# Optimization experiments

Hardware: AMD Instinct MI355X
Metric: run time of the kernel (lower is better)

The kernel has to match this reference:

```python
import jax, jax.numpy as jnp
import numpy as np

NEG_SLOPE = 0.2
BN_EPS = 1e-5


def gat_conv(x, W_src, W_dst, att_src, att_dst, bias, src, dst, num_nodes):
    # PyG GATConv, heads=1, concat=True, self-loops already included in (src,dst)
    h_src = x @ W_src                      # [N, H]
    h_dst = x @ W_dst                      # [N, H]
    a_src = h_src @ att_src                # [N]
    a_dst = h_dst @ att_dst                # [N]
    e = jax.nn.leaky_relu(a_src[src] + a_dst[dst], NEG_SLOPE)   # [E]
    # segment softmax over incoming edges of each dst node
    m = jax.ops.segment_max(e, dst, num_segments=num_nodes)     # [N]
    p = jnp.exp(e - m[dst])
    denom = jax.ops.segment_sum(p, dst, num_segments=num_nodes) # [N]
    alpha = p / denom[dst]                                      # [E]
    msgs = alpha[:, None] * h_src[src]                           # [E, H]
    out = jax.ops.segment_sum(msgs, dst, num_segments=num_nodes)
    return out + bias


def setup_inputs() -> dict:
    key = jax.random.key(0)
    ks = jax.random.split(key, 20)
    N, D_IN, H1, H2, FC, C = 100000, 256, 128, 128, 64, 40
    E = 1600000
    inp = {}
    inp['x'] = jax.random.normal(ks[0], (N, D_IN), dtype=jnp.float32)
    inp['edge_index'] = jax.random.randint(ks[1], (2, E), 0, N, dtype=jnp.int64)
    s = 1.0 / np.sqrt(D_IN)
    inp['W1_src'] = jax.random.uniform(ks[2], (D_IN, H1), jnp.float32, -s, s)
    inp['W1_dst'] = jax.random.uniform(ks[3], (D_IN, H1), jnp.float32, -s, s)
    inp['att1_src'] = jax.random.normal(ks[4], (H1,), jnp.float32) * 0.1
    inp['att1_dst'] = jax.random.normal(ks[5], (H1,), jnp.float32) * 0.1
    inp['b1'] = jnp.zeros((H1,), jnp.float32)
    s = 1.0 / np.sqrt(H1)
    inp['W2_src'] = jax.random.uniform(ks[6], (H1, H2), jnp.float32, -s, s)
    inp['W2_dst'] = jax.random.uniform(ks[7], (H1, H2), jnp.float32, -s, s)
    inp['att2_src'] = jax.random.normal(ks[8], (H2,), jnp.float32) * 0.1
    inp['att2_dst'] = jax.random.normal(ks[9], (H2,), jnp.float32) * 0.1
    inp['b2'] = jnp.zeros((H2,), jnp.float32)
    s = 1.0 / np.sqrt(H2)
    inp['fc1_w'] = jax.random.uniform(ks[10], (H2, FC), jnp.float32, -s, s)
    inp['fc1_b'] = jax.random.uniform(ks[11], (FC,), jnp.float32, -s, s)
    inp['gamma'] = jnp.ones((FC,), jnp.float32)
    inp['beta'] = jnp.zeros((FC,), jnp.float32)
    s = 1.0 / np.sqrt(FC)
    inp['fc2_w'] = jax.random.uniform(ks[12], (FC, C), jnp.float32, -s, s)
    inp['fc2_b'] = jax.random.uniform(ks[13], (C,), jnp.float32, -s, s)
    return inp


def reference(x, edge_index, W1_src, W1_dst, att1_src, att1_dst, b1,
              W2_src, W2_dst, att2_src, att2_dst, b2,
              fc1_w, fc1_b, gamma, beta, fc2_w, fc2_b):
    N = x.shape[0]
    loops = jnp.arange(N, dtype=edge_index.dtype)
    src = jnp.concatenate([edge_index[0], loops])
    dst = jnp.concatenate([edge_index[1], loops])
    h = jax.nn.relu(gat_conv(x, W1_src, W1_dst, att1_src, att1_dst, b1, src, dst, N))
    h = jax.nn.relu(gat_conv(h, W2_src, W2_dst, att2_src, att2_dst, b2, src, dst, N))
    h = h @ fc1_w + fc1_b                   # [N, 64]
    mu = jnp.mean(h, axis=0)
    var = jnp.var(h, axis=0)
    h = (h - mu) * jax.lax.rsqrt(var + BN_EPS) * gamma + beta
    h = jax.nn.relu(h)
    h = h @ fc2_w + fc2_b                   # [N, C]
    return jax.nn.log_softmax(h, axis=-1)
```

## Files before the change

### kernel.cpp

```cpp
#include <hip/hip_runtime.h>
#include <cstddef>

#define LSLOPE 0.2f
#define BN_EPS 1e-5f

__device__ __forceinline__ float lrelu(float x) { return x > 0.f ? x : LSLOPE * x; }

using half4 = __attribute__((ext_vector_type(4))) _Float16;
using half8 = __attribute__((ext_vector_type(8))) _Float16;
using f32x4 = __attribute__((ext_vector_type(4))) float;

struct h2 { _Float16 h, l; };
__device__ __forceinline__ h2 split2h(float x) {
  h2 r;
  r.h = (_Float16)x;
  r.l = (_Float16)(x - (float)r.h);
  return r;
}

__device__ __forceinline__ unsigned short f2bf(float x) {
  unsigned u = __float_as_uint(x);
  unsigned r = (u + 0x7fffu + ((u >> 16) & 1u)) >> 16;
  return (unsigned short)r;
}
__device__ __forceinline__ float bflo(unsigned int u) { return __uint_as_float(u << 16); }
__device__ __forceinline__ float bfhi(unsigned int u) { return __uint_as_float(u & 0xffff0000u); }

__device__ __forceinline__ void bfrag_body(const float* __restrict__ B, _Float16* __restrict__ bh,
                                           _Float16* __restrict__ bl, int K, int M, int t) {
  int KB = K >> 5;
  int lane = t & 63;
  int ckb  = t >> 6;
  int c  = ckb / KB, kb = ckb % KB;
  int mr = lane & 15, quad = lane >> 4;
  int col = c * 16 + mr;
  size_t obase = (size_t)t * 8;
#pragma unroll
  for (int j = 0; j < 8; ++j) {
    int k = kb * 32 + quad * 8 + j;
    h2 s = split2h(B[(size_t)k * M + col]);
    bh[obase + j] = s.h;
    bl[obase + j] = s.l;
  }
}

__device__ __forceinline__ void matvec_body(const float* __restrict__ A, const float* __restrict__ v,
                                            float* __restrict__ out, int R, int K, int t) {
  int w = t >> 6;
  int lane = t & 63;
  if (w >= R) return;
  const float* row = A + (size_t)w * K;
  float s = 0.f;
  for (int k = lane; k < K; k += 64) s = fmaf(row[k], v[k], s);
#pragma unroll
  for (int off = 32; off; off >>= 1) s += __shfl_xor(s, off, 64);
  if (lane == 0) out[w] = s;
}

__global__ __launch_bounds__(256) void prep_k(const float* __restrict__ W1s, const float* __restrict__ W2s,
                                              const float* __restrict__ fc1w,
                                              const float* __restrict__ W1d, const float* __restrict__ att1d,
                                              const float* __restrict__ W2d, const float* __restrict__ att2d,
                                              const float* __restrict__ att1s, const float* __restrict__ att2s,
                                              _Float16* B1h, _Float16* B1l, _Float16* B2h, _Float16* B2l,
                                              _Float16* Bfh, _Float16* Bfl,
                                              float* wvd1, float* wvd2, float* wvs1, float* wvs2) {
  int b = blockIdx.x;
  int tid = threadIdx.x;
  if (b < 16)       bfrag_body(W1s, B1h, B1l, 256, 128, b * 256 + tid);
  else if (b < 24)  bfrag_body(W2s, B2h, B2l, 128, 128, (b - 16) * 256 + tid);
  else if (b < 28)  bfrag_body(fc1w, Bfh, Bfl, 128, 64, (b - 24) * 256 + tid);
  else if (b < 92)  matvec_body(W1d, att1d, wvd1, 256, 128, (b - 28) * 256 + tid);
  else if (b < 124) matvec_body(W2d, att2d, wvd2, 128, 128, (b - 92) * 256 + tid);
  else if (b < 188) matvec_body(W1s, att1s, wvs1, 256, 128, (b - 124) * 256 + tid);
  else              matvec_body(W2s, att2s, wvs2, 128, 128, (b - 188) * 256 + tid);
}

template<int K, int MCOLS, bool PS>
__global__ __launch_bounds__(256) void gemm_dk(const float* __restrict__ Af,
                                               const _Float16* __restrict__ Ah,
                                               const _Float16* __restrict__ Al,
                                               const _Float16* __restrict__ Bh,
                                               const _Float16* __restrict__ Bl,
                                               float* __restrict__ Cf,
                                               unsigned short* __restrict__ Cbf,
                                               const float* __restrict__ wvs,
                                               float* __restrict__ asrc,
                                               const float* __restrict__ wvd,
                                               float* __restrict__ adout,
                                               int N,
                                               const float* __restrict__ bias) {
  constexpr int KB   = K / 32;
  constexpr int HALF = MCOLS / 2;
  constexpr int CT   = HALF / 16;
  const int tid  = threadIdx.x;
  const int wv   = tid >> 6;
  const int wm   = wv >> 1;
  const int wn   = wv & 1;
  const int lane = tid & 63;
  const int quad = lane >> 4;
  const int mr   = lane & 15;
  const int row0 = blockIdx.x * 64;

  int rowr[2];
  bool rok[2];
#pragma unroll
  for (int r = 0; r < 2; ++r) {
    rowr[r] = row0 + wm * 32 + r * 16 + mr;
    rok[r]  = rowr[r] < N;
  }

  f32x4 acc[2][CT];
#pragma unroll
  for (int r = 0; r < 2; ++r)
#pragma unroll
    for (int c = 0; c < CT; ++c) acc[r][c] = (f32x4){0.f, 0.f, 0.f, 0.f};
  float pas[2] = {0.f, 0.f}, pad[2] = {0.f, 0.f};

  const size_t cstride = (size_t)KB * 512;
  const _Float16* bbh = Bh + (size_t)(wn * CT) * cstride + (size_t)lane * 8;
  const _Float16* bbl = Bl + (size_t)(wn * CT) * cstride + (size_t)lane * 8;
  const float4 zf4 = make_float4(0.f, 0.f, 0.f, 0.f);
  const half8 hz = {(_Float16)0, (_Float16)0, (_Float16)0, (_Float16)0,
                    (_Float16)0, (_Float16)0, (_Float16)0, (_Float16)0};

#pragma unroll
  for (int kb = 0; kb < KB; ++kb) {
    const int kk = kb * 32;
    half8 ah[2], al[2];
#pragma unroll
    for (int r = 0; r < 2; ++r) {
      if (PS) {
        const size_t go = (size_t)rowr[r] * K + kk + quad * 8;
        ah[r] = rok[r] ? *(const half8*)&Ah[go] : hz;
        al[r] = rok[r] ? *(const half8*)&Al[go] : hz;
      } else {
        const float* ap = Af + (size_t)rowr[r] * K + kk + quad * 8;
        float4 f0 = rok[r] ? *(const float4*)ap : zf4;
        float4 f1 = rok[r] ? *(const float4*)(ap + 4) : zf4;
        h2 s0 = split2h(f0.x), s1 = split2h(f0.y), s2 = split2h(f0.z), s3 = split2h(f0.w);
        h2 s4 = split2h(f1.x), s5 = split2h(f1.y), s6 = split2h(f1.z), s7 = split2h(f1.w);
        half8 h, l;
        h[0] = s0.h; h[1] = s1.h; h[2] = s2.h; h[3] = s3.h;
        h[4] = s4.h; h[5] = s5.h; h[6] = s6.h; h[7] = s7.h;
        l[0] = s0.l; l[1] = s1.l; l[2] = s2.l; l[3] = s3.l;
        l[4] = s4.l; l[5] = s5.l; l[6] = s6.l; l[7] = s7.l;
        ah[r] = h;
        al[r] = l;
      }
    }
    if (wn == 0 && (wvs || wvd)) {
#pragma unroll
      for (int j = 0; j < 8; ++j) {
        const float vs = wvs ? wvs[kk + quad * 8 + j] : 0.f;
        const float vd = wvd ? wvd[kk + quad * 8 + j] : 0.f;
#pragma unroll
        for (int r = 0; r < 2; ++r) {
          const float av = (float)ah[r][j] + (float)al[r][j];
          if (wvs) pas[r] = fmaf(av, vs, pas[r]);
          if (wvd) pad[r] = fmaf(av, vd, pad[r]);
        }
      }
    }
#pragma unroll
    for (int c = 0; c < CT; ++c) {
      const half8 bh = *(const half8*)&bbh[(size_t)kb * 512 + (size_t)c * cstride];
      const half8 bl = *(const half8*)&bbl[(size_t)kb * 512 + (size_t)c * cstride];
#pragma unroll
      for (int r = 0; r < 2; ++r) {
        f32x4 a = acc[r][c];
        a = __builtin_amdgcn_mfma_f32_16x16x32_f16(al[r], bh, a, 0, 0, 0);
        a = __builtin_amdgcn_mfma_f32_16x16x32_f16(ah[r], bl, a, 0, 0, 0);
        a = __builtin_amdgcn_mfma_f32_16x16x32_f16(ah[r], bh, a, 0, 0, 0);
        acc[r][c] = a;
      }
    }
  }

#pragma unroll
  for (int r = 0; r < 2; ++r)
#pragma unroll
    for (int c = 0; c < CT; ++c) {
      const int gcol = wn * HALF + c * 16 + mr;
      const float bv = bias ? bias[gcol] : 0.f;
#pragma unroll
      for (int q = 0; q < 4; ++q) {
        const int grow = row0 + wm * 32 + r * 16 + quad * 4 + q;
        if (grow < N) {
          float val = acc[r][c][q] + bv;
          if (Cf)  Cf[(size_t)grow * MCOLS + gcol] = val;
          if (Cbf) Cbf[(size_t)grow * 128 + gcol] = f2bf(val);
        }
      }
    }
  if (wn == 0 && wvs) {
#pragma unroll
    for (int r = 0; r < 2; ++r) {
      float d = pas[r];
      d += __shfl_xor(d, 16, 64);
      d += __shfl_xor(d, 32, 64);
      const int grow = row0 + wm * 32 + r * 16 + mr;
      if (quad == 0 && grow < N) asrc[grow] = d;
    }
  }
  if (wn == 0 && wvd) {
#pragma unroll
    for (int r = 0; r < 2; ++r) {
      float d = pad[r];
      d += __shfl_xor(d, 16, 64);
      d += __shfl_xor(d, 32, 64);
      const int grow = row0 + wm * 32 + r * 16 + mr;
      if (quad == 0 && grow < N) adout[grow] = d;
    }
  }
}

__global__ void deg_count_k(const int* __restrict__ edst, int E, int N, int* __restrict__ deg) {
  int i = blockIdx.x * 256 + threadIdx.x;
  if (i >= E + N) return;
  int d = (i < E) ? edst[i] : (i - E);
  atomicAdd(&deg[d], 1);
}

__global__ __launch_bounds__(1024) void scan1_k(const int* __restrict__ deg, int n,
                                                int* __restrict__ ex, int* __restrict__ bsum) {
  __shared__ int sm[1024];
  int t = threadIdx.x;
  int idx = blockIdx.x * 1024 + t;
  int v = (idx < n) ? deg[idx] : 0;
  sm[t] = v;
  __syncthreads();
  for (int off = 1; off < 1024; off <<= 1) {
    int tv = (t >= off) ? sm[t - off] : 0;
    __syncthreads();
    sm[t] += tv;
    __syncthreads();
  }
  if (idx < n) ex[idx] = sm[t] - v;
  if (t == 1023) bsum[blockIdx.x] = sm[t];
}

__global__ void scan3_k(int* __restrict__ ex, const int* __restrict__ bsum, int n, int nb, int total,
                        int* __restrict__ cursor) {
  __shared__ int pbase[2];
  int idx = blockIdx.x * 256 + threadIdx.x;
  int bin0 = (blockIdx.x * 256) >> 10;
  if (threadIdx.x < 2) {
    int b = bin0 + threadIdx.x;
    int s = 0;
    for (int i = 0; i < b && i < nb; ++i) s += bsum[i];
    pbase[threadIdx.x] = s;
  }
  __syncthreads();
  if (idx < n) {
    int v = ex[idx] + pbase[(idx >> 10) - bin0];
    ex[idx] = v;
    cursor[idx] = v;
  }
  if (idx == 0) ex[n] = total;
}

__global__ void scatter_range_k(const int* __restrict__ esrc, const int* __restrict__ edst,
                                int E, int N, int d0, int d1,
                                int* __restrict__ cursor, int* __restrict__ csr_src) {
  int i = blockIdx.x * 256 + threadIdx.x;
  if (i >= E + N) return;
  int d = (i < E) ? edst[i] : (i - E);
  if (d < d0 || d >= d1) return;
  int s = (i < E) ? esrc[i] : d;
  int pos = atomicAdd(&cursor[d], 1);
  csr_src[pos] = s;
}

__global__ __launch_bounds__(256) void gat_agg_k(const unsigned short* __restrict__ hbf,
                                                 const float* __restrict__ a_src,
                                                 const float* __restrict__ a_dst, const int* __restrict__ rowstart,
                                                 const int* __restrict__ csr_src, const float* __restrict__ bias,
                                                 _Float16* __restrict__ oh, _Float16* __restrict__ ol,
                                                 const float* __restrict__ wvd, float* __restrict__ ad_out,
                                                 int N) {
  int w = (blockIdx.x * blockDim.x + threadIdx.x) >> 6;
  int lane = threadIdx.x & 63;
  if (w >= N) return;
  int s0 = rowstart[w];
  int s1 = rowstart[w + 1];
  int deg = s1 - s0;
  float ad = a_dst[w];

  int sA = 0;
  float eA = -3.0e38f;
  if (lane < deg) {
    sA = csr_src[s0 + lane];
    eA = lrelu(a_src[sA] + ad);
  }
  float m = eA;
  for (int j = s0 + 64 + lane; j < s1; j += 64) {
    int s = csr_src[j];
    m = fmaxf(m, lrelu(a_src[s] + ad));
  }
#pragma unroll
  for (int off = 32; off; off >>= 1) m = fmaxf(m, __shfl_xor(m, off, 64));

  float preg = (lane < deg) ? __expf(eA - m) : 0.f;
  float den = preg;
  for (int j = s0 + 64 + lane; j < s1; j += 64) {
    int s = csr_src[j];
    den += __expf(lrelu(a_src[s] + ad) - m);
  }
#pragma unroll
  for (int off = 32; off; off >>= 1) den += __shfl_xor(den, off, 64);
  float inv = 1.f / den;

  const int q  = lane >> 4;
  const int sl = lane & 15;
  const uint4* hrow4 = (const uint4*)hbf;
  float acc[8];
#pragma unroll
  for (int i = 0; i < 8; ++i) acc[i] = 0.f;

  int lim  = deg < 64 ? deg : 64;
  int lim4 = (lim + 3) & ~3;
  for (int jj = 0; jj < lim4; jj += 4) {
    int e = jj + q;
    int s = __shfl(sA, e, 64);
    float wgt = __shfl(preg, e, 64) * inv;
    uint4 u = hrow4[(size_t)s * 16 + sl];
    acc[0] = fmaf(wgt, bflo(u.x), acc[0]);
    acc[1] = fmaf(wgt, bfhi(u.x), acc[1]);
    acc[2] = fmaf(wgt, bflo(u.y), acc[2]);
    acc[3] = fmaf(wgt, bfhi(u.y), acc[3]);
    acc[4] = fmaf(wgt, bflo(u.z), acc[4]);
    acc[5] = fmaf(wgt, bfhi(u.z), acc[5]);
    acc[6] = fmaf(wgt, bflo(u.w), acc[6]);
    acc[7] = fmaf(wgt, bfhi(u.w), acc[7]);
  }
  for (int j = s0 + 64 + q; j < s1; j += 4) {
    int s = csr_src[j];
    float wgt = __expf(lrelu(a_src[s] + ad) - m) * inv;
    uint4 u = hrow4[(size_t)s * 16 + sl];
    acc[0] = fmaf(wgt, bflo(u.x), acc[0]);
    acc[1] = fmaf(wgt, bfhi(u.x), acc[1]);
    acc[2] = fmaf(wgt, bflo(u.y), acc[2]);
    acc[3] = fmaf(wgt, bfhi(u.y), acc[3]);
    acc[4] = fmaf(wgt, bflo(u.z), acc[4]);
    acc[5] = fmaf(wgt, bfhi(u.z), acc[5]);
    acc[6] = fmaf(wgt, bflo(u.w), acc[6]);
    acc[7] = fmaf(wgt, bfhi(u.w), acc[7]);
  }
#pragma unroll
  for (int i = 0; i < 8; ++i) {
    acc[i] += __shfl_xor(acc[i], 16, 64);
    acc[i] += __shfl_xor(acc[i], 32, 64);
  }
  if (q == 0) {
    float4 b0 = *(const float4*)&bias[8 * sl];
    float4 b1 = *(const float4*)&bias[8 * sl + 4];
    float v[8];
    v[0] = fmaxf(acc[0] + b0.x, 0.f);
    v[1] = fmaxf(acc[1] + b0.y, 0.f);
    v[2] = fmaxf(acc[2] + b0.z, 0.f);
    v[3] = fmaxf(acc[3] + b0.w, 0.f);
    v[4] = fmaxf(acc[4] + b1.x, 0.f);
    v[5] = fmaxf(acc[5] + b1.y, 0.f);
    v[6] = fmaxf(acc[6] + b1.z, 0.f);
    v[7] = fmaxf(acc[7] + b1.w, 0.f);
    half8 vh, vl;
#pragma unroll
    for (int i = 0; i < 8; ++i) {
      h2 s = split2h(v[i]);
      vh[i] = s.h;
      vl[i] = s.l;
    }
    size_t base = (size_t)w * 128 + 8 * sl;
    *(half8*)&oh[base] = vh;
    *(half8*)&ol[base] = vl;
    if (wvd) {
      float4 w0 = *(const float4*)&wvd[8 * sl];
      float4 w1 = *(const float4*)&wvd[8 * sl + 4];
      float dd = v[0] * w0.x + v[1] * w0.y + v[2] * w0.z + v[3] * w0.w
               + v[4] * w1.x + v[5] * w1.y + v[6] * w1.z + v[7] * w1.w;
      dd += __shfl_xor(dd, 1, 64);
      dd += __shfl_xor(dd, 2, 64);
      dd += __shfl_xor(dd, 4, 64);
      dd += __shfl_xor(dd, 8, 64);
      if (sl == 0) ad_out[w] = dd;
    }
  }
}

__global__ __launch_bounds__(256) void bn_stats_k(const float* __restrict__ z, int N,
                                                  float* __restrict__ sums, float* __restrict__ sumsq) {
  __shared__ float ls[256], lq[256];
  int col = threadIdx.x & 63;
  int rg = threadIdx.x >> 6;
  float s = 0.f, q = 0.f;
  for (int r = blockIdx.x * 4 + rg; r < N; r += gridDim.x * 4) {
    float v = z[(size_t)r * 64 + col];
    s += v;
    q = fmaf(v, v, q);
  }
  ls[threadIdx.x] = s;
  lq[threadIdx.x] = q;
  __syncthreads();
  if (threadIdx.x < 64) {
    s = ls[col] + ls[col + 64] + ls[col + 128] + ls[col + 192];
    q = lq[col] + lq[col + 64] + lq[col + 128] + lq[col + 192];
    atomicAdd(&sums[col], s);
    atomicAdd(&sumsq[col], q);
  }
}

__global__ __launch_bounds__(256) void fc2_lsm_k(const float* __restrict__ z,
                                                 const float* __restrict__ sums, const float* __restrict__ sumsq,
                                                 const float* __restrict__ gamma, const float* __restrict__ beta,
                                                 const float* __restrict__ w,
                                                 const float* __restrict__ b, float* __restrict__ out,
                                                 int N, float invN) {
  __shared__ float ssc[64], ssh[64];
  if (threadIdx.x < 64) {
    int c = threadIdx.x;
    float mean = sums[c] * invN;
    float var = sumsq[c] * invN - mean * mean;
    float rs = rsqrtf(var + BN_EPS);
    float sc = gamma[c] * rs;
    ssc[c] = sc;
    ssh[c] = beta[c] - mean * sc;
  }
  __syncthreads();
  int n = blockIdx.x * 256 + threadIdx.x;
  if (n >= N) return;
  float o[40];
#pragma unroll
  for (int c = 0; c < 40; ++c) o[c] = b[c];
  const float* zr = z + (size_t)n * 64;
  for (int k = 0; k < 64; ++k) {
    float v = fmaxf(fmaf(zr[k], ssc[k], ssh[k]), 0.f);
#pragma unroll
    for (int c = 0; c < 40; ++c) o[c] = fmaf(v, w[k * 40 + c], o[c]);
  }
  float mx = o[0];
#pragma unroll
  for (int c = 1; c < 40; ++c) mx = fmaxf(mx, o[c]);
  float s = 0.f;
#pragma unroll
  for (int c = 0; c < 40; ++c) s += __expf(o[c] - mx);
  float ls = __logf(s);
  float* orow = out + (size_t)n * 40;
#pragma unroll
  for (int c = 0; c < 40; ++c) orow[c] = o[c] - mx - ls;
}

static inline char* al16(char* p) { return (char*)(((size_t)p + 15) & ~(size_t)15); }

extern "C" void kernel_launch(void* const* d_in, const int* in_sizes, int n_in,
                              void* d_out, int out_size, void* d_ws, size_t ws_size,
                              hipStream_t stream) {
  const float* x     = (const float*)d_in[0];
  const int*   eidx  = (const int*)d_in[1];
  const float* W1s   = (const float*)d_in[2];
  const float* W1d   = (const float*)d_in[3];
  const float* att1s = (const float*)d_in[4];
  const float* att1d = (const float*)d_in[5];
  const float* b1    = (const float*)d_in[6];
  const float* W2s   = (const float*)d_in[7];
  const float* W2d   = (const float*)d_in[8];
  const float* att2s = (const float*)d_in[9];
  const float* att2d = (const float*)d_in[10];
  const float* b2    = (const float*)d_in[11];
  const float* fc1w  = (const float*)d_in[12];
  const float* fc1b  = (const float*)d_in[13];
  const float* gamma = (const float*)d_in[14];
  const float* beta  = (const float*)d_in[15];
  const float* fc2w  = (const float*)d_in[16];
  const float* fc2b  = (const float*)d_in[17];
  float* out = (float*)d_out;

  const int N  = in_sizes[0] / 256;
  const int E  = in_sizes[1] / 2;
  const int ET = E + N;

  char* p = (char*)d_ws;
  int* deg      = (int*)p;     p += (size_t)N * 4;
  float* sums   = (float*)p;   p += 64 * 4;
  float* sumsq  = (float*)p;   p += 64 * 4;
  unsigned short* bhA = (unsigned short*)p; p += (size_t)N * 128 * 2;
  _Float16* hAh = (_Float16*)p;  p += (size_t)N * 128 * 2;
  _Float16* hAl = (_Float16*)p;  p += (size_t)N * 128 * 2;
  float* hF = (float*)p;         p += (size_t)N * 64 * 4;
  int* rowstart = (int*)p;     p += (size_t)(N + 1) * 4;
  int* cursor   = (int*)p;     p += (size_t)N * 4;
  int* csr_src  = (int*)p;     p += (size_t)ET * 4;
  float* a_src  = (float*)p;   p += (size_t)N * 4;
  float* a_dst  = (float*)p;   p += (size_t)N * 4;
  float* a_dst2 = (float*)p;   p += (size_t)N * 4;
  float* wvd1   = (float*)p;   p += 256 * 4;
  float* wvd2   = (float*)p;   p += 128 * 4;
  float* wvs1   = (float*)p;   p += 256 * 4;
  float* wvs2   = (float*)p;   p += 128 * 4;
  int* bsum     = (int*)p;     p += 256 * 4;
  p = al16(p);
  _Float16* B1h = (_Float16*)p; p += (size_t)256 * 128 * 2;
  _Float16* B1l = (_Float16*)p; p += (size_t)256 * 128 * 2;
  _Float16* B2h = (_Float16*)p; p += (size_t)128 * 128 * 2;
  _Float16* B2l = (_Float16*)p; p += (size_t)128 * 128 * 2;
  _Float16* Bfh = (_Float16*)p; p += (size_t)128 * 64 * 2;
  _Float16* Bfl = (_Float16*)p; p += (size_t)128 * 64 * 2;

  const int* esrc = eidx;
  const int* edst = eidx + E;

  hipMemsetAsync(deg, 0, (size_t)N * 4 + 512, stream);

  deg_count_k<<<(ET + 255) / 256, 256, 0, stream>>>(edst, E, N, deg);
  int nb = (N + 1023) / 1024;
  scan1_k<<<nb, 1024, 0, stream>>>(deg, N, rowstart, bsum);
  scan3_k<<<(N + 255) / 256, 256, 0, stream>>>(rowstart, bsum, N, nb, ET, cursor);
  {
    const int NR = 8;
    int step = (N + NR - 1) / NR;
    for (int r = 0; r < NR; ++r) {
      int d0 = r * step;
      int d1 = d0 + step < N ? d0 + step : N;
      scatter_range_k<<<(ET + 255) / 256, 256, 0, stream>>>(esrc, edst, E, N, d0, d1, cursor, csr_src);
    }
  }

  prep_k<<<220, 256, 0, stream>>>(W1s, W2s, fc1w, W1d, att1d, W2d, att2d, att1s, att2s,
                                  B1h, B1l, B2h, B2l, Bfh, Bfl, wvd1, wvd2, wvs1, wvs2);

  const int gdk = (N + 63) / 64;

  gemm_dk<256, 128, false><<<gdk, 256, 0, stream>>>(x, nullptr, nullptr, B1h, B1l,
                                                    nullptr, bhA, wvs1, a_src, wvd1, a_dst, N, nullptr);
  gat_agg_k<<<(N + 3) / 4, 256, 0, stream>>>(bhA, a_src, a_dst, rowstart, csr_src, b1,
                                             hAh, hAl, wvd2, a_dst2, N);

  gemm_dk<128, 128, true><<<gdk, 256, 0, stream>>>(nullptr, hAh, hAl, B2h, B2l,
                                                   nullptr, bhA, wvs2, a_src, nullptr, nullptr, N, nullptr);
  gat_agg_k<<<(N + 3) / 4, 256, 0, stream>>>(bhA, a_src, a_dst2, rowstart, csr_src, b2,
                                             hAh, hAl, nullptr, nullptr, N);

  gemm_dk<128, 64, true><<<gdk, 256, 0, stream>>>(nullptr, hAh, hAl, Bfh, Bfl,
                                                  hF, nullptr, nullptr, nullptr, nullptr, nullptr, N, fc1b);
  bn_stats_k<<<512, 256, 0, stream>>>(hF, N, sums, sumsq);
  fc2_lsm_k<<<(N + 255) / 256, 256, 0, stream>>>(hF, sums, sumsq, gamma, beta, fc2w, fc2b, out,
                                                 N, 1.0f / (float)N);
}
```

Baseline: 761.5 us.

## Stage A tiles through double-buffered LDS in dense GEMM kernels

The GEMM kernel now loads each 64x32 A tile cooperatively into shared memory, swizzled to avoid bank conflicts, instead of each wave reading its rows directly from global memory. Loads for the next k-block are issued into registers and written to a second LDS buffer while MFMAs run on the current one. For the fp32 first layer, the hi/lo fp16 split is also done once per element instead of by both column-half waves. This adds LDS traffic and a barrier per k-step, and the loop is no longer explicitly unrolled.

```diff
diff --git a/kernel.cpp b/kernel.cpp
--- a/kernel.cpp
+++ b/kernel.cpp
@@ -77,7 +77,7 @@
 }
 
 template<int K, int MCOLS, bool PS>
-__global__ __launch_bounds__(256) void gemm_dk(const float* __restrict__ Af,
+__global__ __launch_bounds__(256) void gemm_sk(const float* __restrict__ Af,
                                                const _Float16* __restrict__ Ah,
                                                const _Float16* __restrict__ Al,
                                                const _Float16* __restrict__ Bh,
@@ -93,22 +93,16 @@
   constexpr int KB   = K / 32;
   constexpr int HALF = MCOLS / 2;
   constexpr int CT   = HALF / 16;
+  __shared__ __align__(16) _Float16 sAh[2][64 * 32];
+  __shared__ __align__(16) _Float16 sAl[2][64 * 32];
   const int tid  = threadIdx.x;
+  const int row0 = blockIdx.x * 64;
   const int wv   = tid >> 6;
   const int wm   = wv >> 1;
   const int wn   = wv & 1;
   const int lane = tid & 63;
   const int quad = lane >> 4;
   const int mr   = lane & 15;
-  const int row0 = blockIdx.x * 64;
-
-  int rowr[2];
-  bool rok[2];
-#pragma unroll
-  for (int r = 0; r < 2; ++r) {
-    rowr[r] = row0 + wm * 32 + r * 16 + mr;
-    rok[r]  = rowr[r] < N;
-  }
 
   f32x4 acc[2][CT];
 #pragma unroll
@@ -116,38 +110,85 @@
 #pragma unroll
     for (int c = 0; c < CT; ++c) acc[r][c] = (f32x4){0.f, 0.f, 0.f, 0.f};
   float pas[2] = {0.f, 0.f}, pad[2] = {0.f, 0.f};
+
+  int srow, skc, soff;
+  bool sok;
+  if (PS) {
+    srow = tid >> 2;
+    skc  = (tid & 3) << 3;
+  } else {
+    srow = tid >> 3;
+    skc  = (tid & 7) << 2;
+  }
+  soff = srow * 32 + ((skc + srow * 8) & 31);
+  sok  = (row0 + srow) < N;
+  int srow2 = 0, skc2 = 0, soff2 = 0;
+  bool sok2 = false;
+  if (!PS) {
+    int s = tid + 256;
+    srow2 = s >> 3;
+    skc2  = (s & 7) << 2;
+    soff2 = srow2 * 32 + ((skc2 + srow2 * 8) & 31);
+    sok2  = (row0 + srow2) < N;
+  }
+
+  const float4 zf4 = make_float4(0.f, 0.f, 0.f, 0.f);
+  const uint4  zu4 = make_uint4(0u, 0u, 0u, 0u);
+
+  float4 pf0, pf1;
+  uint4 puh, pul;
+  if (PS) {
+    size_t go = (size_t)(row0 + srow) * K + skc;
+    puh = sok ? *(const uint4*)&Ah[go] : zu4;
+    pul = sok ? *(const uint4*)&Al[go] : zu4;
+  } else {
+    pf0 = sok  ? *(const float4*)&Af[(size_t)(row0 + srow) * K + skc]   : zf4;
+    pf1 = sok2 ? *(const float4*)&Af[(size_t)(row0 + srow2) * K + skc2] : zf4;
+  }
+  if (PS) {
+    *(uint4*)&sAh[0][soff] = puh;
+    *(uint4*)&sAl[0][soff] = pul;
+  } else {
+    h2 s0 = split2h(pf0.x), s1 = split2h(pf0.y), s2 = split2h(pf0.z), s3 = split2h(pf0.w);
+    half4 h4, l4;
+    h4[0] = s0.h; h4[1] = s1.h; h4[2] = s2.h; h4[3] = s3.h;
+    l4[0] = s0.l; l4[1] = s1.l; l4[2] = s2.l; l4[3] = s3.l;
+    *(half4*)&sAh[0][soff] = h4;
+    *(half4*)&sAl[0][soff] = l4;
+    h2 t0 = split2h(pf1.x), t1 = split2h(pf1.y), t2 = split2h(pf1.z), t3 = split2h(pf1.w);
+    h4[0] = t0.h; h4[1] = t1.h; h4[2] = t2.h; h4[3] = t3.h;
+    l4[0] = t0.l; l4[1] = t1.l; l4[2] = t2.l; l4[3] = t3.l;
+    *(half4*)&sAh[0][soff2] = h4;
+    *(half4*)&sAl[0][soff2] = l4;
+  }
+  __syncthreads();
 
   const size_t cstride = (size_t)KB * 512;
   const _Float16* bbh = Bh + (size_t)(wn * CT) * cstride + (size_t)lane * 8;
   const _Float16* bbl = Bl + (size_t)(wn * CT) * cstride + (size_t)lane * 8;
-  const float4 zf4 = make_float4(0.f, 0.f, 0.f, 0.f);
-  const half8 hz = {(_Float16)0, (_Float16)0, (_Float16)0, (_Float16)0,
-                    (_Float16)0, (_Float16)0, (_Float16)0, (_Float16)0};
-
-#pragma unroll
+
   for (int kb = 0; kb < KB; ++kb) {
-    const int kk = kb * 32;
+    const int cur = kb & 1, nxt = cur ^ 1;
+    const int kk = kb << 5;
+    if (kb + 1 < KB) {
+      const int kn = (kb + 1) << 5;
+      if (PS) {
+        size_t go = (size_t)(row0 + srow) * K + kn + skc;
+        puh = sok ? *(const uint4*)&Ah[go] : zu4;
+        pul = sok ? *(const uint4*)&Al[go] : zu4;
+      } else {
+        pf0 = sok  ? *(const float4*)&Af[(size_t)(row0 + srow) * K + kn + skc]   : zf4;
+        pf1 = sok2 ? *(const float4*)&Af[(size_t)(row0 + srow2) * K + kn + skc2] : zf4;
+      }
+    }
+
     half8 ah[2], al[2];
 #pragma unroll
     for (int r = 0; r < 2; ++r) {
-      if (PS) {
-        const size_t go = (size_t)rowr[r] * K + kk + quad * 8;
-        ah[r] = rok[r] ? *(const half8*)&Ah[go] : hz;
-        al[r] = rok[r] ? *(const half8*)&Al[go] : hz;
-      } else {
-        const float* ap = Af + (size_t)rowr[r] * K + kk + quad * 8;
-        float4 f0 = rok[r] ? *(const float4*)ap : zf4;
-        float4 f1 = rok[r] ? *(const float4*)(ap + 4) : zf4;
-        h2 s0 = split2h(f0.x), s1 = split2h(f0.y), s2 = split2h(f0.z), s3 = split2h(f0.w);
-        h2 s4 = split2h(f1.x), s5 = split2h(f1.y), s6 = split2h(f1.z), s7 = split2h(f1.w);
-        half8 h, l;
-        h[0] = s0.h; h[1] = s1.h; h[2] = s2.h; h[3] = s3.h;
-        h[4] = s4.h; h[5] = s5.h; h[6] = s6.h; h[7] = s7.h;
-        l[0] = s0.l; l[1] = s1.l; l[2] = s2.l; l[3] = s3.l;
-        l[4] = s4.l; l[5] = s5.l; l[6] = s6.l; l[7] = s7.l;
-        ah[r] = h;
-        al[r] = l;
-      }
+      int row = wm * 32 + r * 16 + mr;
+      int off = row * 32 + ((quad + row) & 3) * 8;
+      ah[r] = *(const half8*)&sAh[cur][off];
+      al[r] = *(const half8*)&sAl[cur][off];
     }
     if (wn == 0 && (wvs || wvd)) {
 #pragma unroll
@@ -175,6 +216,25 @@
         acc[r][c] = a;
       }
     }
+    if (kb + 1 < KB) {
+      if (PS) {
+        *(uint4*)&sAh[nxt][soff] = puh;
+        *(uint4*)&sAl[nxt][soff] = pul;
+      } else {
+        h2 s0 = split2h(pf0.x), s1 = split2h(pf0.y), s2 = split2h(pf0.z), s3 = split2h(pf0.w);
+        half4 h4, l4;
+        h4[0] = s0.h; h4[1] = s1.h; h4[2] = s2.h; h4[3] = s3.h;
+        l4[0] = s0.l; l4[1] = s1.l; l4[2] = s2.l; l4[3] = s3.l;
+        *(half4*)&sAh[nxt][soff] = h4;
+        *(half4*)&sAl[nxt][soff] = l4;
+        h2 t0 = split2h(pf1.x), t1 = split2h(pf1.y), t2 = split2h(pf1.z), t3 = split2h(pf1.w);
+        h4[0] = t0.h; h4[1] = t1.h; h4[2] = t2.h; h4[3] = t3.h;
+        l4[0] = t0.l; l4[1] = t1.l; l4[2] = t2.l; l4[3] = t3.l;
+        *(half4*)&sAh[nxt][soff2] = h4;
+        *(half4*)&sAl[nxt][soff2] = l4;
+      }
+    }
+    __syncthreads();
   }
 
 #pragma unroll
@@ -530,17 +590,17 @@
 
   const int gdk = (N + 63) / 64;
 
-  gemm_dk<256, 128, false><<<gdk, 256, 0, stream>>>(x, nullptr, nullptr, B1h, B1l,
+  gemm_sk<256, 128, false><<<gdk, 256, 0, stream>>>(x, nullptr, nullptr, B1h, B1l,
                                                     nullptr, bhA, wvs1, a_src, wvd1, a_dst, N, nullptr);
   gat_agg_k<<<(N + 3) / 4, 256, 0, stream>>>(bhA, a_src, a_dst, rowstart, csr_src, b1,
                                              hAh, hAl, wvd2, a_dst2, N);
 
-  gemm_dk<128, 128, true><<<gdk, 256, 0, stream>>>(nullptr, hAh, hAl, B2h, B2l,
+  gemm_sk<128, 128, true><<<gdk, 256, 0, stream>>>(nullptr, hAh, hAl, B2h, B2l,
                                                    nullptr, bhA, wvs2, a_src, nullptr, nullptr, N, nullptr);
   gat_agg_k<<<(N + 3) / 4, 256, 0, stream>>>(bhA, a_src, a_dst2, rowstart, csr_src, b2,
                                              hAh, hAl, nullptr, nullptr, N);
 
-  gemm_dk<128, 64, true><<<gdk, 256, 0, stream>>>(nullptr, hAh, hAl, Bfh, Bfl,
+  gemm_sk<128, 64, true><<<gdk, 256, 0, stream>>>(nullptr, hAh, hAl, Bfh, Bfl,
                                                   hF, nullptr, nullptr, nullptr, nullptr, nullptr, N, fc1b);
   bn_stats_k<<<512, 256, 0, stream>>>(hF, N, sums, sumsq);
   fc2_lsm_k<<<(N + 255) / 256, 256, 0, stream>>>(hF, sums, sumsq, gamma, beta, fc2w, fc2b, out,
```

Measured after the change: 687.9 us. 1.11x faster.

## Stage A tile in swizzled LDS and reorder B fragments kb-major in GEMMs

Applied to the files above, without the earlier changes.

The dense GEMM kernels now load the 64-row A tile cooperatively with coalesced 16-byte loads into XOR-swizzled shared memory (fp16 hi/lo split), then read MFMA fragments from LDS. Previously each wave read strided rows from global memory directly. The B fragment layout is also reordered so that all column tiles for one k-block are contiguous. The aim is better global coalescing and less redundant A traffic, at the cost of large LDS use (64 KB for K=256), which can reduce occupancy.

```diff
diff --git a/kernel.cpp b/kernel.cpp
--- a/kernel.cpp
+++ b/kernel.cpp
@@ -29,12 +29,13 @@
 __device__ __forceinline__ void bfrag_body(const float* __restrict__ B, _Float16* __restrict__ bh,
                                            _Float16* __restrict__ bl, int K, int M, int t) {
   int KB = K >> 5;
+  int CTF = M >> 4;
   int lane = t & 63;
   int ckb  = t >> 6;
   int c  = ckb / KB, kb = ckb % KB;
   int mr = lane & 15, quad = lane >> 4;
   int col = c * 16 + mr;
-  size_t obase = (size_t)t * 8;
+  size_t obase = ((size_t)kb * CTF + c) * 512 + (size_t)lane * 8;
 #pragma unroll
   for (int j = 0; j < 8; ++j) {
     int k = kb * 32 + quad * 8 + j;
@@ -77,7 +78,7 @@
 }
 
 template<int K, int MCOLS, bool PS>
-__global__ __launch_bounds__(256) void gemm_dk(const float* __restrict__ Af,
+__global__ __launch_bounds__(256) void gemm_nb(const float* __restrict__ Af,
                                                const _Float16* __restrict__ Ah,
                                                const _Float16* __restrict__ Al,
                                                const _Float16* __restrict__ Bh,
@@ -91,53 +92,41 @@
                                                int N,
                                                const float* __restrict__ bias) {
   constexpr int KB   = K / 32;
+  constexpr int CTF  = MCOLS / 16;
   constexpr int HALF = MCOLS / 2;
   constexpr int CT   = HALF / 16;
+  __shared__ __align__(16) _Float16 sAh[64 * K];
+  __shared__ __align__(16) _Float16 sAl[64 * K];
   const int tid  = threadIdx.x;
+  const int row0 = blockIdx.x * 64;
   const int wv   = tid >> 6;
   const int wm   = wv >> 1;
   const int wn   = wv & 1;
   const int lane = tid & 63;
   const int quad = lane >> 4;
   const int mr   = lane & 15;
-  const int row0 = blockIdx.x * 64;
-
-  int rowr[2];
-  bool rok[2];
-#pragma unroll
-  for (int r = 0; r < 2; ++r) {
-    rowr[r] = row0 + wm * 32 + r * 16 + mr;
-    rok[r]  = rowr[r] < N;
-  }
-
-  f32x4 acc[2][CT];
-#pragma unroll
-  for (int r = 0; r < 2; ++r)
-#pragma unroll
-    for (int c = 0; c < CT; ++c) acc[r][c] = (f32x4){0.f, 0.f, 0.f, 0.f};
-  float pas[2] = {0.f, 0.f}, pad[2] = {0.f, 0.f};
-
-  const size_t cstride = (size_t)KB * 512;
-  const _Float16* bbh = Bh + (size_t)(wn * CT) * cstride + (size_t)lane * 8;
-  const _Float16* bbl = Bl + (size_t)(wn * CT) * cstride + (size_t)lane * 8;
+
   const float4 zf4 = make_float4(0.f, 0.f, 0.f, 0.f);
-  const half8 hz = {(_Float16)0, (_Float16)0, (_Float16)0, (_Float16)0,
-                    (_Float16)0, (_Float16)0, (_Float16)0, (_Float16)0};
-
-#pragma unroll
-  for (int kb = 0; kb < KB; ++kb) {
-    const int kk = kb * 32;
-    half8 ah[2], al[2];
-#pragma unroll
-    for (int r = 0; r < 2; ++r) {
+  const uint4  zu4 = make_uint4(0u, 0u, 0u, 0u);
+
+  {
+    const int ar = tid >> 2;
+    const int ac = tid & 3;
+    const bool aok = (row0 + ar) < N;
+#pragma unroll
+    for (int i = 0; i < K / 32; ++i) {
+      const int c8 = ac + i * 4;
+      const int sx = c8 ^ (ar & 7);
       if (PS) {
-        const size_t go = (size_t)rowr[r] * K + kk + quad * 8;
-        ah[r] = rok[r] ? *(const half8*)&Ah[go] : hz;
-        al[r] = rok[r] ? *(const half8*)&Al[go] : hz;
+        const size_t go = (size_t)(row0 + ar) * K + c8 * 8;
+        uint4 uh = aok ? *(const uint4*)&Ah[go] : zu4;
+        uint4 ul = aok ? *(const uint4*)&Al[go] : zu4;
+        *(uint4*)&sAh[ar * K + sx * 8] = uh;
+        *(uint4*)&sAl[ar * K + sx * 8] = ul;
       } else {
-        const float* ap = Af + (size_t)rowr[r] * K + kk + quad * 8;
-        float4 f0 = rok[r] ? *(const float4*)ap : zf4;
-        float4 f1 = rok[r] ? *(const float4*)(ap + 4) : zf4;
+        const float* ap = &Af[(size_t)(row0 + ar) * K + c8 * 8];
+        float4 f0 = aok ? *(const float4*)ap : zf4;
+        float4 f1 = aok ? *(const float4*)(ap + 4) : zf4;
         h2 s0 = split2h(f0.x), s1 = split2h(f0.y), s2 = split2h(f0.z), s3 = split2h(f0.w);
         h2 s4 = split2h(f1.x), s5 = split2h(f1.y), s6 = split2h(f1.z), s7 = split2h(f1.w);
         half8 h, l;
@@ -145,9 +134,30 @@
         h[4] = s4.h; h[5] = s5.h; h[6] = s6.h; h[7] = s7.h;
         l[0] = s0.l; l[1] = s1.l; l[2] = s2.l; l[3] = s3.l;
         l[4] = s4.l; l[5] = s5.l; l[6] = s6.l; l[7] = s7.l;
-        ah[r] = h;
-        al[r] = l;
+        *(half8*)&sAh[ar * K + sx * 8] = h;
+        *(half8*)&sAl[ar * K + sx * 8] = l;
       }
+    }
+  }
+  __syncthreads();
+
+  f32x4 acc[2][CT];
+#pragma unroll
+  for (int r = 0; r < 2; ++r)
+#pragma unroll
+    for (int c = 0; c < CT; ++c) acc[r][c] = (f32x4){0.f, 0.f, 0.f, 0.f};
+  float pas[2] = {0.f, 0.f}, pad[2] = {0.f, 0.f};
+
+#pragma unroll
+  for (int kb = 0; kb < KB; ++kb) {
+    const int kk = kb << 5;
+    half8 ah[2], al[2];
+#pragma unroll
+    for (int r = 0; r < 2; ++r) {
+      const int row = wm * 32 + r * 16 + mr;
+      const int sx = (kb * 4 + quad) ^ (row & 7);
+      ah[r] = *(const half8*)&sAh[row * K + sx * 8];
+      al[r] = *(const half8*)&sAl[row * K + sx * 8];
     }
     if (wn == 0 && (wvs || wvd)) {
 #pragma unroll
@@ -164,8 +174,9 @@
     }
 #pragma unroll
     for (int c = 0; c < CT; ++c) {
-      const half8 bh = *(const half8*)&bbh[(size_t)kb * 512 + (size_t)c * cstride];
-      const half8 bl = *(const half8*)&bbl[(size_t)kb * 512 + (size_t)c * cstride];
+      const size_t bo = ((size_t)kb * CTF + wn * CT + c) * 512 + (size_t)lane * 8;
+      const half8 bh = *(const half8*)&Bh[bo];
+      const half8 bl = *(const half8*)&Bl[bo];
 #pragma unroll
       for (int r = 0; r < 2; ++r) {
         f32x4 a = acc[r][c];
@@ -530,17 +541,17 @@
 
   const int gdk = (N + 63) / 64;
 
-  gemm_dk<256, 128, false><<<gdk, 256, 0, stream>>>(x, nullptr, nullptr, B1h, B1l,
+  gemm_nb<256, 128, false><<<gdk, 256, 0, stream>>>(x, nullptr, nullptr, B1h, B1l,
                                                     nullptr, bhA, wvs1, a_src, wvd1, a_dst, N, nullptr);
   gat_agg_k<<<(N + 3) / 4, 256, 0, stream>>>(bhA, a_src, a_dst, rowstart, csr_src, b1,
                                              hAh, hAl, wvd2, a_dst2, N);
 
-  gemm_dk<128, 128, true><<<gdk, 256, 0, stream>>>(nullptr, hAh, hAl, B2h, B2l,
+  gemm_nb<128, 128, true><<<gdk, 256, 0, stream>>>(nullptr, hAh, hAl, B2h, B2l,
                                                    nullptr, bhA, wvs2, a_src, nullptr, nullptr, N, nullptr);
   gat_agg_k<<<(N + 3) / 4, 256, 0, stream>>>(bhA, a_src, a_dst2, rowstart, csr_src, b2,
                                              hAh, hAl, nullptr, nullptr, N);
 
-  gemm_dk<128, 64, true><<<gdk, 256, 0, stream>>>(nullptr, hAh, hAl, Bfh, Bfl,
+  gemm_nb<128, 64, true><<<gdk, 256, 0, stream>>>(nullptr, hAh, hAl, Bfh, Bfl,
                                                   hF, nullptr, nullptr, nullptr, nullptr, nullptr, N, fc1b);
   bn_stats_k<<<512, 256, 0, stream>>>(hF, N, sums, sumsq);
   fc2_lsm_k<<<(N + 255) / 256, 256, 0, stream>>>(hF, sums, sumsq, gamma, beta, fc2w, fc2b, out,
```

New measurement: 715.9 us. 1.06x faster.
